# Kernel optimization log

Hardware: AMD Instinct MI355X
Metric: run time of the kernel (lower is better)

The kernel has to match this reference:

```python
import jax, jax.numpy as jnp
import numpy as np

N, IN, OUT, F = 8192, 128, 128, 2
P_EDGE = 0.004  # ~32 neighbors per row


def _sparse_lap(k1, k2):
    mask = jax.random.uniform(k1, (N, N)) < P_EDGE
    mask = mask | jnp.eye(N, dtype=bool)  # nonzero diagonal, like a Laplacian
    vals = jax.random.normal(k2, (N, N), dtype=jnp.float32)
    return jnp.where(mask, vals, 0.0)


def setup_inputs() -> dict:
    key = jax.random.key(0)
    ks = jax.random.split(key, 11)
    x = jax.random.normal(ks[0], (N, IN), dtype=jnp.float32)
    lap_up = _sparse_lap(ks[1], ks[2])
    lap_down = _sparse_lap(ks[3], ks[4])
    proj = jax.random.normal(ks[5], (N, N), dtype=jnp.float32) * np.float32(1.0 / np.sqrt(N))
    scale = np.float32(1.0 / np.sqrt(IN))
    W_up = jax.random.normal(ks[6], (F, IN, OUT), dtype=jnp.float32) * scale
    W_down = jax.random.normal(ks[7], (F, IN, OUT), dtype=jnp.float32) * scale
    a_up = jax.random.normal(ks[8], (2 * OUT * F,), dtype=jnp.float32) * np.float32(0.1)
    a_down = jax.random.normal(ks[9], (2 * OUT * F,), dtype=jnp.float32) * np.float32(0.1)
    W_har = jax.random.normal(ks[10], (IN, OUT), dtype=jnp.float32) * scale
    return dict(x=x, laplacian_up=lap_up, laplacian_down=lap_down, projection_mat=proj,
                W_up=W_up, a_up=a_up, W_down=W_down, a_down=a_down, W_har=W_har)


def _san_conv(x, neighborhood, W, a):
    # W: [F, in, out]; a: [2*out*F]
    n = x.shape[0]
    f, _, out = W.shape
    z = jnp.einsum('ni,fio->fno', x, W)                      # [F, N, out] (x @ weight)
    z_r = jnp.transpose(z, (1, 0, 2)).reshape(n, f * out)    # permute(1,0,2).reshape
    a_src, a_tgt = a[: f * out], a[f * out:]                 # cat([source_j, target_i]) @ a
    s = z_r @ a_src                                          # [N] per-source term
    t = z_r @ a_tgt                                          # [N] per-target term
    mask = neighborhood != 0                                 # sparse pattern of laplacian
    logits = jnp.where(mask, jax.nn.elu(t[:, None] + s[None, :]), -jnp.inf)
    att = jnp.where(mask, jax.nn.softmax(logits, axis=1), 0.0)  # sparse softmax over dim=1
    # sum_{p=1}^{F} att^p @ z[p-1]
    out_msg = jnp.zeros((n, out), dtype=x.dtype)
    A = att
    for p in range(f):
        out_msg = out_msg + A @ z[p]
        if p + 1 < f:
            A = A @ att
    return out_msg


def reference(x, laplacian_up, laplacian_down, projection_mat, W_up, a_up, W_down, a_down, W_har):
    z_down = _san_conv(x, laplacian_down, W_down, a_down)
    z_up = _san_conv(x, laplacian_up, W_up, a_up)
    z_har = projection_mat @ (x @ W_har)
    return z_down + z_up + z_har
```

## Files before the change

### kernel.cpp

```cpp
#include <hip/hip_runtime.h>

#define NN 8192
#define CAP 128

typedef __attribute__((ext_vector_type(8))) short bf16x8;
typedef __attribute__((ext_vector_type(4))) float f32x4;

__device__ __forceinline__ short f2bf(float f) {
    unsigned u = __builtin_bit_cast(unsigned, f);
    u += 0x7FFFu + ((u >> 16) & 1u);
    return (short)(u >> 16);
}

__global__ __launch_bounds__(256) void k_small_gemm(
        const float* __restrict__ x, const float* __restrict__ Wdown,
        const float* __restrict__ Wup, const float* __restrict__ Whar,
        float* __restrict__ zbuf) {
    int wsel = blockIdx.y;
    const float* W = (wsel == 0) ? Wdown : (wsel == 1) ? Wdown + 16384 :
                     (wsel == 2) ? Wup   : (wsel == 3) ? Wup + 16384 : Whar;
    float* out = zbuf + (size_t)wsel * NN * 128;
    __shared__ float Wl[128 * 128];
    __shared__ float Xl[32 * 128];
    int tid = threadIdx.x;
    int row0 = blockIdx.x * 32;
    const float4* W4 = (const float4*)W;
    float4* Wl4 = (float4*)Wl;
    for (int i = tid; i < 4096; i += 256) Wl4[i] = W4[i];
    const float4* X4 = (const float4*)(x + (size_t)row0 * 128);
    float4* Xl4 = (float4*)Xl;
    for (int i = tid; i < 1024; i += 256) Xl4[i] = X4[i];
    __syncthreads();
    int tx = tid & 31, ty = tid >> 5;
    float acc[4][4] = {};
#pragma unroll 2
    for (int i = 0; i < 128; ++i) {
        float w0 = Wl[i * 128 + tx];
        float w1 = Wl[i * 128 + tx + 32];
        float w2 = Wl[i * 128 + tx + 64];
        float w3 = Wl[i * 128 + tx + 96];
#pragma unroll
        for (int rr = 0; rr < 4; ++rr) {
            float xv = Xl[(ty * 4 + rr) * 128 + i];
            acc[rr][0] += xv * w0; acc[rr][1] += xv * w1;
            acc[rr][2] += xv * w2; acc[rr][3] += xv * w3;
        }
    }
#pragma unroll
    for (int rr = 0; rr < 4; ++rr) {
        float* o = out + (size_t)(row0 + ty * 4 + rr) * 128 + tx;
        o[0] = acc[rr][0]; o[32] = acc[rr][1]; o[64] = acc[rr][2]; o[96] = acc[rr][3];
    }
}

__global__ __launch_bounds__(256) void k_st(
        const float* __restrict__ zbuf, const float* __restrict__ a_down,
        const float* __restrict__ a_up, float* __restrict__ stbuf) {
    int sel = blockIdx.y;
    const float* z0 = zbuf + (size_t)sel * 2 * NN * 128;
    const float* z1 = z0 + (size_t)NN * 128;
    const float* a = sel ? a_up : a_down;
    int row = ((int)blockIdx.x * 256 + (int)threadIdx.x) >> 6;
    int lane = threadIdx.x & 63;
    float z0a = z0[(size_t)row * 128 + lane], z0b = z0[(size_t)row * 128 + lane + 64];
    float z1a = z1[(size_t)row * 128 + lane], z1b = z1[(size_t)row * 128 + lane + 64];
    float ps = z0a * a[lane]       + z0b * a[lane + 64]
             + z1a * a[128 + lane] + z1b * a[192 + lane];
    float pt = z0a * a[256 + lane] + z0b * a[320 + lane]
             + z1a * a[384 + lane] + z1b * a[448 + lane];
    for (int off = 32; off; off >>= 1) {
        ps += __shfl_xor(ps, off);
        pt += __shfl_xor(pt, off);
    }
    if (lane == 0) {
        stbuf[(size_t)sel * 2 * NN + row] = ps;
        stbuf[(size_t)sel * 2 * NN + NN + row] = pt;
    }
}

__global__ __launch_bounds__(256) void k_scan(
        const float* __restrict__ lapdown, const float* __restrict__ lapup,
        int* __restrict__ cntbuf, int* __restrict__ colbuf) {
    int sel = blockIdx.y;
    const float* lap = sel ? lapup : lapdown;
    int row = ((int)blockIdx.x * 256 + (int)threadIdx.x) >> 6;
    int lane = threadIdx.x & 63;
    const float4* lr = (const float4*)(lap + (size_t)row * NN);
    int* crow = colbuf + (size_t)sel * NN * CAP + (size_t)row * CAP;
    unsigned long long ltmask = (1ull << lane) - 1ull;
    int c = 0;
    for (int it = 0; it < 32; ++it) {
        float4 v = lr[it * 64 + lane];
#pragma unroll
        for (int q = 0; q < 4; ++q) {
            float f = (q == 0) ? v.x : (q == 1) ? v.y : (q == 2) ? v.z : v.w;
            bool nz = (f != 0.0f);
            unsigned long long m = __ballot(nz);
            if (nz) {
                int slot = c + __popcll(m & ltmask);
                if (slot < CAP) crow[slot] = it * 256 + lane * 4 + q;
            }
            c += __popcll(m);
        }
    }
    int cc = (c < CAP) ? c : CAP;
    int cpad = (cc + 7) & ~7;
    if (lane < cpad - cc) crow[cc + lane] = 0;
    if (lane == 0) cntbuf[sel * NN + row] = cc;
}

__global__ __launch_bounds__(256) void k_att(
        const float* __restrict__ stbuf, const int* __restrict__ cntbuf,
        const int* __restrict__ colbuf, float* __restrict__ valbuf) {
    int sel = blockIdx.y;
    const float* s = stbuf + (size_t)sel * 2 * NN;
    const float* t = s + NN;
    int row = ((int)blockIdx.x * 256 + (int)threadIdx.x) >> 6;
    int lane = threadIdx.x & 63;
    int c = cntbuf[sel * NN + row];
    const int* cr = colbuf + (size_t)sel * NN * CAP + (size_t)row * CAP;
    float* vr = valbuf + (size_t)sel * NN * CAP + (size_t)row * CAP;
    float tv = t[row];
    float e0 = -1e30f, e1 = -1e30f;
    if (lane < c)      { float v = tv + s[cr[lane]];      e0 = v > 0.f ? v : expm1f(v); }
    if (lane + 64 < c) { float v = tv + s[cr[lane + 64]]; e1 = v > 0.f ? v : expm1f(v); }
    float m = fmaxf(e0, e1);
    for (int off = 32; off; off >>= 1) m = fmaxf(m, __shfl_xor(m, off));
    float p0 = (lane < c)      ? expf(e0 - m) : 0.f;
    float p1 = (lane + 64 < c) ? expf(e1 - m) : 0.f;
    float sum = p0 + p1;
    for (int off = 32; off; off >>= 1) sum += __shfl_xor(sum, off);
    float inv = 1.0f / sum;
    if (lane < c)      vr[lane] = p0 * inv;
    if (lane + 64 < c) vr[lane + 64] = p1 * inv;
    int cpad = (c + 7) & ~7;
    if (lane < cpad - c) vr[c + lane] = 0.f;
}

__global__ __launch_bounds__(512) void k_tr(
        const float* __restrict__ h, unsigned short* __restrict__ hT) {
    __shared__ unsigned short tile[32 * 128];
    int tid = threadIdx.x;
    int k0 = blockIdx.x * 32;
    int r = tid >> 4;
    int c0 = (tid & 15) * 8;
    const float4* src = (const float4*)(h + (size_t)(k0 + r) * 128 + c0);
    float4 a = src[0], b = src[1];
    unsigned short* tp = &tile[r * 128 + c0];
    tp[0] = (unsigned short)f2bf(a.x); tp[1] = (unsigned short)f2bf(a.y);
    tp[2] = (unsigned short)f2bf(a.z); tp[3] = (unsigned short)f2bf(a.w);
    tp[4] = (unsigned short)f2bf(b.x); tp[5] = (unsigned short)f2bf(b.y);
    tp[6] = (unsigned short)f2bf(b.z); tp[7] = (unsigned short)f2bf(b.w);
    __syncthreads();
    int c = tid & 127;
    int seg = tid >> 7;
    unsigned short v[8];
#pragma unroll
    for (int i = 0; i < 8; ++i) v[i] = tile[(seg * 8 + i) * 128 + c];
    uint4 pack;
    pack.x = (unsigned)v[0] | ((unsigned)v[1] << 16);
    pack.y = (unsigned)v[2] | ((unsigned)v[3] << 16);
    pack.z = (unsigned)v[4] | ((unsigned)v[5] << 16);
    pack.w = (unsigned)v[6] | ((unsigned)v[7] << 16);
    *(uint4*)(hT + (size_t)c * NN + k0 + seg * 8) = pack;
}

__global__ __launch_bounds__(256) void k_proj(
        const float* __restrict__ P, const unsigned short* __restrict__ hT,
        float* __restrict__ partial, int lgnks) {
    int gw = ((int)blockIdx.x * 256 + (int)threadIdx.x) >> 6;
    int lane = threadIdx.x & 63;
    int nksm1 = (1 << lgnks) - 1;
    int strip = gw >> lgnks;
    int ks = gw & nksm1;
    int kiters = 256 >> lgnks;
    int row0 = strip * 16;
    int k0 = ks << (13 - lgnks);
    int l15 = lane & 15;
    int koff = (lane >> 4) * 8;
    const float* A = P + (size_t)(row0 + l15) * NN + k0 + koff;
    const unsigned short* B0 = hT + (size_t)l15 * NN + k0 + koff;
    f32x4 acc[8];
#pragma unroll
    for (int i = 0; i < 8; ++i) acc[i] = (f32x4){0.f, 0.f, 0.f, 0.f};
    float4 a0 = *(const float4*)(A);
    float4 a1 = *(const float4*)(A + 4);
    for (int kc = 0; kc < kiters; ++kc) {
        float4 n0, n1;
        if (kc + 1 < kiters) {
            const float* An = A + 32 * (kc + 1);
            n0 = *(const float4*)(An);
            n1 = *(const float4*)(An + 4);
        }
        bf16x8 af;
        af[0] = f2bf(a0.x); af[1] = f2bf(a0.y); af[2] = f2bf(a0.z); af[3] = f2bf(a0.w);
        af[4] = f2bf(a1.x); af[5] = f2bf(a1.y); af[6] = f2bf(a1.z); af[7] = f2bf(a1.w);
        const unsigned short* Bp = B0 + kc * 32;
#pragma unroll
        for (int ct = 0; ct < 8; ++ct) {
            bf16x8 bf = *(const bf16x8*)(Bp + (size_t)ct * 16 * NN);
            acc[ct] = __builtin_amdgcn_mfma_f32_16x16x32_bf16(af, bf, acc[ct], 0, 0, 0);
        }
        a0 = n0; a1 = n1;
    }
    float* out = partial + (size_t)ks * NN * 128;
    int prow = row0 + (lane >> 4) * 4;
#pragma unroll
    for (int ct = 0; ct < 8; ++ct)
#pragma unroll
        for (int r = 0; r < 4; ++r)
            out[(size_t)(prow + r) * 128 + ct * 16 + l15] = acc[ct][r];
}

__device__ __forceinline__ void edge_acc(
        int c, const int* __restrict__ cr, const float* __restrict__ vr,
        const float* __restrict__ B, int lane, float& ax, float& ay) {
    int cpad = (c + 7) & ~7;
    for (int e = 0; e < cpad; e += 8) {
        int4   j0 = *(const int4*)(cr + e);
        int4   j1 = *(const int4*)(cr + e + 4);
        float4 v0 = *(const float4*)(vr + e);
        float4 v1 = *(const float4*)(vr + e + 4);
        float2 b0 = ((const float2*)(B + (size_t)j0.x * 128))[lane];
        float2 b1 = ((const float2*)(B + (size_t)j0.y * 128))[lane];
        float2 b2 = ((const float2*)(B + (size_t)j0.z * 128))[lane];
        float2 b3 = ((const float2*)(B + (size_t)j0.w * 128))[lane];
        float2 b4 = ((const float2*)(B + (size_t)j1.x * 128))[lane];
        float2 b5 = ((const float2*)(B + (size_t)j1.y * 128))[lane];
        float2 b6 = ((const float2*)(B + (size_t)j1.z * 128))[lane];
        float2 b7 = ((const float2*)(B + (size_t)j1.w * 128))[lane];
        ax += v0.x * b0.x; ay += v0.x * b0.y;
        ax += v0.y * b1.x; ay += v0.y * b1.y;
        ax += v0.z * b2.x; ay += v0.z * b2.y;
        ax += v0.w * b3.x; ay += v0.w * b3.y;
        ax += v1.x * b4.x; ay += v1.x * b4.y;
        ax += v1.y * b5.x; ay += v1.y * b5.y;
        ax += v1.z * b6.x; ay += v1.z * b6.y;
        ax += v1.w * b7.x; ay += v1.w * b7.y;
    }
}

__global__ __launch_bounds__(256) void k_pass1(
        const int* __restrict__ cnt, const int* __restrict__ col,
        const float* __restrict__ val, const float* __restrict__ zbuf,
        float* __restrict__ wbuf) {
    int sel = blockIdx.y;
    const float* z0 = zbuf + (size_t)sel * 2 * NN * 128;
    const float* z1 = z0 + (size_t)NN * 128;
    float* w = wbuf + (size_t)sel * NN * 128;
    int row = ((int)blockIdx.x * 256 + (int)threadIdx.x) >> 6;
    int lane = threadIdx.x & 63;
    int c = cnt[sel * NN + row];
    float2 a = ((const float2*)(z0 + (size_t)row * 128))[lane];
    float ax = a.x, ay = a.y;
    edge_acc(c, col + ((size_t)sel * NN + row) * CAP,
             val + ((size_t)sel * NN + row) * CAP, z1, lane, ax, ay);
    ((float2*)(w + (size_t)row * 128))[lane] = make_float2(ax, ay);
}

__global__ __launch_bounds__(256) void k_final(
        const int* __restrict__ cnt, const int* __restrict__ col,
        const float* __restrict__ val, const float* __restrict__ wbuf,
        const float* __restrict__ partial, int nks, float* __restrict__ out) {
    int row = ((int)blockIdx.x * 256 + (int)threadIdx.x) >> 6;
    int lane = threadIdx.x & 63;
    float ax = 0.f, ay = 0.f;
    for (int ks = 0; ks < nks; ++ks) {
        float2 p = ((const float2*)(partial + (size_t)ks * NN * 128 + (size_t)row * 128))[lane];
        ax += p.x; ay += p.y;
    }
    edge_acc(cnt[row], col + (size_t)row * CAP, val + (size_t)row * CAP,
             wbuf, lane, ax, ay);
    edge_acc(cnt[NN + row], col + ((size_t)NN + row) * CAP,
             val + ((size_t)NN + row) * CAP, wbuf + (size_t)NN * 128, lane, ax, ay);
    ((float2*)(out + (size_t)row * 128))[lane] = make_float2(ax, ay);
}

extern "C" void kernel_launch(void* const* d_in, const int* in_sizes, int n_in,
                              void* d_out, int out_size, void* d_ws, size_t ws_size,
                              hipStream_t stream) {
    const float* x        = (const float*)d_in[0];
    const float* lap_up   = (const float*)d_in[1];
    const float* lap_down = (const float*)d_in[2];
    const float* proj     = (const float*)d_in[3];
    const float* W_up     = (const float*)d_in[4];
    const float* a_up     = (const float*)d_in[5];
    const float* W_down   = (const float*)d_in[6];
    const float* a_down   = (const float*)d_in[7];
    const float* W_har    = (const float*)d_in[8];
    float* out = (float*)d_out;
    float* ws = (float*)d_ws;

    const size_t ZSZ = (size_t)NN * 128;
    const size_t fixed = 5 * ZSZ + 4 * NN + 2 * NN + 2 * ZSZ + 2 * ZSZ
                       + 2 * ZSZ + ZSZ / 2;
    int lgnks = 4;
    while (lgnks > 2 && (fixed + ((size_t)1 << lgnks) * ZSZ) * 4 > ws_size) --lgnks;
    int nks = 1 << lgnks;

    size_t off = 0;
    float* zbuf = ws + off;              off += 5 * ZSZ;
    float* stbuf = ws + off;             off += 4 * NN;
    int* cntbuf = (int*)(ws + off);      off += 2 * NN;
    int* colbuf = (int*)(ws + off);      off += 2 * ZSZ;
    float* valbuf = ws + off;            off += 2 * ZSZ;
    float* wbuf = ws + off;              off += 2 * ZSZ;
    unsigned short* hT = (unsigned short*)(ws + off); off += ZSZ / 2;
    float* partial = ws + off;           off += (size_t)nks * ZSZ;

    hipLaunchKernelGGL(k_small_gemm, dim3(256, 5), dim3(256), 0, stream,
                       x, W_down, W_up, W_har, zbuf);
    hipLaunchKernelGGL(k_st, dim3(2048, 2), dim3(256), 0, stream,
                       zbuf, a_down, a_up, stbuf);
    hipLaunchKernelGGL(k_scan, dim3(2048, 2), dim3(256), 0, stream,
                       lap_down, lap_up, cntbuf, colbuf);
    hipLaunchKernelGGL(k_att, dim3(2048, 2), dim3(256), 0, stream,
                       stbuf, cntbuf, colbuf, valbuf);
    hipLaunchKernelGGL(k_tr, dim3(256), dim3(512), 0, stream,
                       zbuf + 4 * ZSZ, hT);
    hipLaunchKernelGGL(k_proj, dim3(128 * nks), dim3(256), 0, stream,
                       proj, hT, partial, lgnks);
    hipLaunchKernelGGL(k_pass1, dim3(2048, 2), dim3(256), 0, stream,
                       cntbuf, colbuf, valbuf, zbuf, wbuf);
    hipLaunchKernelGGL(k_final, dim3(2048), dim3(256), 0, stream,
                       cntbuf, colbuf, valbuf, wbuf, partial, nks, out);
}
```

Measured before the change: 936.5 us.

## Tile projection GEMM through double-buffered LDS and fuse scan with attention

The projection GEMM now stages 64x64 fp32 tiles of P and 128x64 bf16 tiles of hT in double-buffered shared memory. Four waves share the B operand instead of each reading it from global memory, and the k-split is fixed at 4. The sparse scan and attention softmax kernels are merged, so column indices are kept in shared memory rather than re-read from global. The trade-off is a coarser grid with fewer blocks per CU, plus a block barrier on every k step.

```diff
diff --git a/kernel.cpp b/kernel.cpp
--- a/kernel.cpp
+++ b/kernel.cpp
@@ -2,6 +2,8 @@
 
 #define NN 8192
 #define CAP 128
+#define PLDA 68
+#define PLDB 72
 
 typedef __attribute__((ext_vector_type(8))) short bf16x8;
 typedef __attribute__((ext_vector_type(4))) float f32x4;
@@ -78,15 +80,20 @@
     }
 }
 
-__global__ __launch_bounds__(256) void k_scan(
+__global__ __launch_bounds__(256) void k_scanatt(
         const float* __restrict__ lapdown, const float* __restrict__ lapup,
-        int* __restrict__ cntbuf, int* __restrict__ colbuf) {
+        const float* __restrict__ stbuf,
+        int* __restrict__ cntbuf, int* __restrict__ colbuf,
+        float* __restrict__ valbuf) {
+    __shared__ int colsh[4][CAP];
     int sel = blockIdx.y;
     const float* lap = sel ? lapup : lapdown;
-    int row = ((int)blockIdx.x * 256 + (int)threadIdx.x) >> 6;
+    int wid = threadIdx.x >> 6;
+    int row = (int)blockIdx.x * 4 + wid;
     int lane = threadIdx.x & 63;
     const float4* lr = (const float4*)(lap + (size_t)row * NN);
     int* crow = colbuf + (size_t)sel * NN * CAP + (size_t)row * CAP;
+    int* csh = colsh[wid];
     unsigned long long ltmask = (1ull << lane) - 1ull;
     int c = 0;
     for (int it = 0; it < 32; ++it) {
@@ -98,7 +105,11 @@
             unsigned long long m = __ballot(nz);
             if (nz) {
                 int slot = c + __popcll(m & ltmask);
-                if (slot < CAP) crow[slot] = it * 256 + lane * 4 + q;
+                if (slot < CAP) {
+                    int cidx = it * 256 + lane * 4 + q;
+                    crow[slot] = cidx;
+                    csh[slot] = cidx;
+                }
             }
             c += __popcll(m);
         }
@@ -107,34 +118,23 @@
     int cpad = (cc + 7) & ~7;
     if (lane < cpad - cc) crow[cc + lane] = 0;
     if (lane == 0) cntbuf[sel * NN + row] = cc;
-}
-
-__global__ __launch_bounds__(256) void k_att(
-        const float* __restrict__ stbuf, const int* __restrict__ cntbuf,
-        const int* __restrict__ colbuf, float* __restrict__ valbuf) {
-    int sel = blockIdx.y;
     const float* s = stbuf + (size_t)sel * 2 * NN;
     const float* t = s + NN;
-    int row = ((int)blockIdx.x * 256 + (int)threadIdx.x) >> 6;
-    int lane = threadIdx.x & 63;
-    int c = cntbuf[sel * NN + row];
-    const int* cr = colbuf + (size_t)sel * NN * CAP + (size_t)row * CAP;
     float* vr = valbuf + (size_t)sel * NN * CAP + (size_t)row * CAP;
     float tv = t[row];
     float e0 = -1e30f, e1 = -1e30f;
-    if (lane < c)      { float v = tv + s[cr[lane]];      e0 = v > 0.f ? v : expm1f(v); }
-    if (lane + 64 < c) { float v = tv + s[cr[lane + 64]]; e1 = v > 0.f ? v : expm1f(v); }
+    if (lane < cc)      { float v = tv + s[csh[lane]];      e0 = v > 0.f ? v : expm1f(v); }
+    if (lane + 64 < cc) { float v = tv + s[csh[lane + 64]]; e1 = v > 0.f ? v : expm1f(v); }
     float m = fmaxf(e0, e1);
     for (int off = 32; off; off >>= 1) m = fmaxf(m, __shfl_xor(m, off));
-    float p0 = (lane < c)      ? expf(e0 - m) : 0.f;
-    float p1 = (lane + 64 < c) ? expf(e1 - m) : 0.f;
+    float p0 = (lane < cc)      ? expf(e0 - m) : 0.f;
+    float p1 = (lane + 64 < cc) ? expf(e1 - m) : 0.f;
     float sum = p0 + p1;
     for (int off = 32; off; off >>= 1) sum += __shfl_xor(sum, off);
     float inv = 1.0f / sum;
-    if (lane < c)      vr[lane] = p0 * inv;
-    if (lane + 64 < c) vr[lane + 64] = p1 * inv;
-    int cpad = (c + 7) & ~7;
-    if (lane < cpad - c) vr[c + lane] = 0.f;
+    if (lane < cc)      vr[lane] = p0 * inv;
+    if (lane + 64 < cc) vr[lane + 64] = p1 * inv;
+    if (lane < cpad - cc) vr[cc + lane] = 0.f;
 }
 
 __global__ __launch_bounds__(512) void k_tr(
@@ -167,44 +167,76 @@
 
 __global__ __launch_bounds__(256) void k_proj(
         const float* __restrict__ P, const unsigned short* __restrict__ hT,
-        float* __restrict__ partial, int lgnks) {
-    int gw = ((int)blockIdx.x * 256 + (int)threadIdx.x) >> 6;
-    int lane = threadIdx.x & 63;
-    int nksm1 = (1 << lgnks) - 1;
-    int strip = gw >> lgnks;
-    int ks = gw & nksm1;
-    int kiters = 256 >> lgnks;
-    int row0 = strip * 16;
-    int k0 = ks << (13 - lgnks);
-    int l15 = lane & 15;
-    int koff = (lane >> 4) * 8;
-    const float* A = P + (size_t)(row0 + l15) * NN + k0 + koff;
-    const unsigned short* B0 = hT + (size_t)l15 * NN + k0 + koff;
+        float* __restrict__ partial) {
+    __shared__ float As[2][64 * PLDA];
+    __shared__ unsigned short Bs[2][128 * PLDB];
+    int tid = threadIdx.x;
+    int strip = (int)blockIdx.x >> 2;
+    int ks = (int)blockIdx.x & 3;
+    int RB = strip * 64;
+    int k0 = ks * 2048;
+    int w = tid >> 6, lane = tid & 63;
+    int l15 = lane & 15, koff = (lane >> 4) * 8;
+    int ar = tid >> 2, ak = (tid & 3) * 16;
+    int bn = tid >> 1, bk = (tid & 1) * 32;
+    const float* Ag = P + (size_t)(RB + ar) * NN + k0 + ak;
+    const unsigned short* Bg = hT + (size_t)bn * NN + k0 + bk;
+    float* Aw0 = &As[0][ar * PLDA + ak];
+    unsigned short* Bw0 = &Bs[0][bn * PLDB + bk];
+    float* Aw1 = &As[1][ar * PLDA + ak];
+    unsigned short* Bw1 = &Bs[1][bn * PLDB + bk];
+
+    float4 sa[4]; uint4 sb[4];
+#pragma unroll
+    for (int i = 0; i < 4; ++i) sa[i] = *(const float4*)(Ag + i * 4);
+#pragma unroll
+    for (int i = 0; i < 4; ++i) sb[i] = *(const uint4*)(Bg + i * 8);
+#pragma unroll
+    for (int i = 0; i < 4; ++i) *(float4*)(Aw0 + i * 4) = sa[i];
+#pragma unroll
+    for (int i = 0; i < 4; ++i) *(uint4*)(Bw0 + i * 8) = sb[i];
+    __syncthreads();
+
     f32x4 acc[8];
 #pragma unroll
     for (int i = 0; i < 8; ++i) acc[i] = (f32x4){0.f, 0.f, 0.f, 0.f};
-    float4 a0 = *(const float4*)(A);
-    float4 a1 = *(const float4*)(A + 4);
-    for (int kc = 0; kc < kiters; ++kc) {
-        float4 n0, n1;
-        if (kc + 1 < kiters) {
-            const float* An = A + 32 * (kc + 1);
-            n0 = *(const float4*)(An);
-            n1 = *(const float4*)(An + 4);
-        }
-        bf16x8 af;
-        af[0] = f2bf(a0.x); af[1] = f2bf(a0.y); af[2] = f2bf(a0.z); af[3] = f2bf(a0.w);
-        af[4] = f2bf(a1.x); af[5] = f2bf(a1.y); af[6] = f2bf(a1.z); af[7] = f2bf(a1.w);
-        const unsigned short* Bp = B0 + kc * 32;
-#pragma unroll
-        for (int ct = 0; ct < 8; ++ct) {
-            bf16x8 bf = *(const bf16x8*)(Bp + (size_t)ct * 16 * NN);
-            acc[ct] = __builtin_amdgcn_mfma_f32_16x16x32_bf16(af, bf, acc[ct], 0, 0, 0);
-        }
-        a0 = n0; a1 = n1;
+
+    for (int t = 0; t < 32; ++t) {
+        int cur = t & 1;
+        if (t + 1 < 32) {
+            const float* Agn = Ag + (t + 1) * 64;
+            const unsigned short* Bgn = Bg + (t + 1) * 64;
+#pragma unroll
+            for (int i = 0; i < 4; ++i) sa[i] = *(const float4*)(Agn + i * 4);
+#pragma unroll
+            for (int i = 0; i < 4; ++i) sb[i] = *(const uint4*)(Bgn + i * 8);
+        }
+#pragma unroll
+        for (int kk = 0; kk < 2; ++kk) {
+            const float* Ab = &As[cur][(w * 16 + l15) * PLDA + kk * 32 + koff];
+            float4 a0 = *(const float4*)Ab;
+            float4 a1 = *(const float4*)(Ab + 4);
+            bf16x8 af;
+            af[0] = f2bf(a0.x); af[1] = f2bf(a0.y); af[2] = f2bf(a0.z); af[3] = f2bf(a0.w);
+            af[4] = f2bf(a1.x); af[5] = f2bf(a1.y); af[6] = f2bf(a1.z); af[7] = f2bf(a1.w);
+#pragma unroll
+            for (int ct = 0; ct < 8; ++ct) {
+                bf16x8 bf = *(const bf16x8*)(&Bs[cur][(ct * 16 + l15) * PLDB + kk * 32 + koff]);
+                acc[ct] = __builtin_amdgcn_mfma_f32_16x16x32_bf16(af, bf, acc[ct], 0, 0, 0);
+            }
+        }
+        if (t + 1 < 32) {
+            float* Aw = (cur ? Aw0 : Aw1);
+            unsigned short* Bw = (cur ? Bw0 : Bw1);
+#pragma unroll
+            for (int i = 0; i < 4; ++i) *(float4*)(Aw + i * 4) = sa[i];
+#pragma unroll
+            for (int i = 0; i < 4; ++i) *(uint4*)(Bw + i * 8) = sb[i];
+        }
+        __syncthreads();
     }
     float* out = partial + (size_t)ks * NN * 128;
-    int prow = row0 + (lane >> 4) * 4;
+    int prow = RB + w * 16 + (lane >> 4) * 4;
 #pragma unroll
     for (int ct = 0; ct < 8; ++ct)
 #pragma unroll
@@ -261,11 +293,12 @@
 __global__ __launch_bounds__(256) void k_final(
         const int* __restrict__ cnt, const int* __restrict__ col,
         const float* __restrict__ val, const float* __restrict__ wbuf,
-        const float* __restrict__ partial, int nks, float* __restrict__ out) {
+        const float* __restrict__ partial, float* __restrict__ out) {
     int row = ((int)blockIdx.x * 256 + (int)threadIdx.x) >> 6;
     int lane = threadIdx.x & 63;
     float ax = 0.f, ay = 0.f;
-    for (int ks = 0; ks < nks; ++ks) {
+#pragma unroll
+    for (int ks = 0; ks < 4; ++ks) {
         float2 p = ((const float2*)(partial + (size_t)ks * NN * 128 + (size_t)row * 128))[lane];
         ax += p.x; ay += p.y;
     }
@@ -292,12 +325,6 @@
     float* ws = (float*)d_ws;
 
     const size_t ZSZ = (size_t)NN * 128;
-    const size_t fixed = 5 * ZSZ + 4 * NN + 2 * NN + 2 * ZSZ + 2 * ZSZ
-                       + 2 * ZSZ + ZSZ / 2;
-    int lgnks = 4;
-    while (lgnks > 2 && (fixed + ((size_t)1 << lgnks) * ZSZ) * 4 > ws_size) --lgnks;
-    int nks = 1 << lgnks;
-
     size_t off = 0;
     float* zbuf = ws + off;              off += 5 * ZSZ;
     float* stbuf = ws + off;             off += 4 * NN;
@@ -306,22 +333,20 @@
     float* valbuf = ws + off;            off += 2 * ZSZ;
     float* wbuf = ws + off;              off += 2 * ZSZ;
     unsigned short* hT = (unsigned short*)(ws + off); off += ZSZ / 2;
-    float* partial = ws + off;           off += (size_t)nks * ZSZ;
+    float* partial = ws + off;           off += 4 * ZSZ;
 
     hipLaunchKernelGGL(k_small_gemm, dim3(256, 5), dim3(256), 0, stream,
                        x, W_down, W_up, W_har, zbuf);
     hipLaunchKernelGGL(k_st, dim3(2048, 2), dim3(256), 0, stream,
                        zbuf, a_down, a_up, stbuf);
-    hipLaunchKernelGGL(k_scan, dim3(2048, 2), dim3(256), 0, stream,
-                       lap_down, lap_up, cntbuf, colbuf);
-    hipLaunchKernelGGL(k_att, dim3(2048, 2), dim3(256), 0, stream,
-                       stbuf, cntbuf, colbuf, valbuf);
+    hipLaunchKernelGGL(k_scanatt, dim3(2048, 2), dim3(256), 0, stream,
+                       lap_down, lap_up, stbuf, cntbuf, colbuf, valbuf);
     hipLaunchKernelGGL(k_tr, dim3(256), dim3(512), 0, stream,
                        zbuf + 4 * ZSZ, hT);
-    hipLaunchKernelGGL(k_proj, dim3(128 * nks), dim3(256), 0, stream,
-                       proj, hT, partial, lgnks);
+    hipLaunchKernelGGL(k_proj, dim3(512), dim3(256), 0, stream,
+                       proj, hT, partial);
     hipLaunchKernelGGL(k_pass1, dim3(2048, 2), dim3(256), 0, stream,
                        cntbuf, colbuf, valbuf, zbuf, wbuf);
     hipLaunchKernelGGL(k_final, dim3(2048), dim3(256), 0, stream,
-                       cntbuf, colbuf, valbuf, wbuf, partial, nks, out);
-}
+                       cntbuf, colbuf, valbuf, wbuf, partial, out);
+}
```

Result: faster. 820.9 us (-12.3%).
